# Optimization experiments

Measured on AMD Instinct MI355X. Metric: run time of the kernel, lower is better.

The kernel has to match this reference:

```python
import jax, jax.numpy as jnp
import numpy as np

B = 262144
HIST = 24
FORE = 20
HID = 256
# torch: tau_int = clamp(tau,1,18).long().item(); default tau=6.0 -> static 6 (host sync in torch)
TAU_INT = 6


def setup_inputs() -> dict:
    key = jax.random.key(0)
    ks = jax.random.split(key, 9)
    s = 0.1
    return {
        "history": jax.random.normal(ks[0], (B, HIST), jnp.float32),
        "enc_w1": jax.random.normal(ks[1], (HIST + FORE, HID), jnp.float32) * s,
        "enc_b1": jnp.zeros((HID,), jnp.float32),
        "enc_w2": jax.random.normal(ks[2], (HID, HID), jnp.float32) * s,
        "enc_b2": jnp.zeros((HID,), jnp.float32),
        "cor_w1": jax.random.normal(ks[3], (HID, HID), jnp.float32) * s,
        "cor_b1": jnp.zeros((HID,), jnp.float32),
        "cor_w2": jax.random.normal(ks[4], (HID, FORE), jnp.float32) * s,
        "cor_b2": jnp.zeros((FORE,), jnp.float32),
        "alpha": jnp.float32(0.2),
        "beta": jnp.float32(0.3),
        "gamma": jnp.float32(0.01),
        "tau": jnp.float32(6.0),
        "lambda_mix": jnp.float32(0.5),
    }


def _physics_core(history, alpha, beta, gamma, steps):
    a = jax.nn.sigmoid(alpha)
    b = jax.nn.sigmoid(beta)
    g = jnp.abs(gamma)
    T0 = history[:, -1]                      # [B]
    buf0 = history[:, -TAU_INT:].T           # [tau, B]; buf0[0] = history[:, -tau]

    def step(carry, _):
        T, buf = carry
        T_delayed = buf[0]
        T_new = T - a * T - b * T_delayed - g * T ** 3
        buf = jnp.concatenate([buf[1:], T_new[None, :]], axis=0)
        return (T_new, buf), T_new

    _, preds = jax.lax.scan(step, (T0, buf0), None, length=steps)
    return preds.T                            # [B, steps]


def reference(history, enc_w1, enc_b1, enc_w2, enc_b2,
              cor_w1, cor_b1, cor_w2, cor_b2,
              alpha, beta, gamma, tau, lambda_mix):
    T_physics = _physics_core(history, alpha, beta, gamma, FORE)   # [B, FORE]
    combined = jnp.concatenate([history, T_physics], axis=1)       # [B, HIST+FORE]
    h = jnp.tanh(combined @ enc_w1 + enc_b1)
    features = jnp.tanh(h @ enc_w2 + enc_b2)
    c = jnp.tanh(features @ cor_w1 + cor_b1)
    T_soft = c @ cor_w2 + cor_b2                                   # [B, FORE]
    lam = jax.nn.sigmoid(lambda_mix)
    T_pred = T_physics + lam * T_soft
    return (T_pred, T_physics, T_soft)
```

## Files before the change

### kernel.cpp

```cpp
#include <hip/hip_runtime.h>
#include <hip/hip_bf16.h>

#define NROWS 262144
#define HISTC 24
#define FOREC 20

typedef __bf16        v8bf __attribute__((ext_vector_type(8)));
typedef float         v4f  __attribute__((ext_vector_type(4)));
typedef unsigned int  v4u  __attribute__((ext_vector_type(4)));
typedef unsigned int  v2u  __attribute__((ext_vector_type(2)));

#define WS_WT1_OFF 64
#define WT1_ELEMS 16384
#define WT2_ELEMS 65536
#define WT3_ELEMS 65536
#define WT4_ELEMS 8192

__device__ __forceinline__ unsigned short f2bf(float x) {
    unsigned u = __builtin_bit_cast(unsigned, x);
    u += 0x7FFFu + ((u >> 16) & 1u);
    return (unsigned short)(u >> 16);
}

__device__ __forceinline__ unsigned pack2bf(float a, float b) {
    unsigned ua = __builtin_bit_cast(unsigned, a);
    unsigned ub = __builtin_bit_cast(unsigned, b);
    ua += 0x7FFFu + ((ua >> 16) & 1u);
    ub += 0x7FFFu + ((ub >> 16) & 1u);
    return (ua >> 16) | (ub & 0xFFFF0000u);
}

__device__ __forceinline__ float fast_tanh(float x) {
    float t = x * 2.885390081777927f;
    float p = __builtin_amdgcn_exp2f(t);
    float r = __builtin_amdgcn_rcpf(p + 1.0f);
    return __builtin_fmaf(-2.0f, r, 1.0f);
}

__global__ void prep_kernel(const float* __restrict__ w1, const float* __restrict__ w2,
                            const float* __restrict__ w3, const float* __restrict__ w4,
                            const float* __restrict__ alpha, const float* __restrict__ beta,
                            const float* __restrict__ gamma, const float* __restrict__ lmix,
                            unsigned char* __restrict__ ws)
{
    if (blockIdx.x == 608) {
        int t = threadIdx.x;
        float* wsf = (float*)ws;
        if (t == 0) wsf[0] = 1.0f / (1.0f + expf(-alpha[0]));
        else if (t == 1) wsf[1] = 1.0f / (1.0f + expf(-beta[0]));
        else if (t == 2) wsf[2] = fabsf(gamma[0]);
        else if (t == 3) wsf[3] = 1.0f / (1.0f + expf(-lmix[0]));
        return;
    }
    int idx = blockIdx.x * 256 + threadIdx.x;
    const float* src;
    int KT, Kreal, Nreal, srcN, local;
    unsigned short* dst = (unsigned short*)(ws + WS_WT1_OFF);
    if (idx < WT1_ELEMS) {
        local = idx; src = w1; KT = 2; Kreal = 44; Nreal = 256; srcN = 256;
    } else if (idx < WT1_ELEMS + WT2_ELEMS) {
        local = idx - WT1_ELEMS; dst += WT1_ELEMS;
        src = w2; KT = 8; Kreal = 256; Nreal = 256; srcN = 256;
    } else if (idx < WT1_ELEMS + WT2_ELEMS + WT3_ELEMS) {
        local = idx - (WT1_ELEMS + WT2_ELEMS); dst += WT1_ELEMS + WT2_ELEMS;
        src = w3; KT = 8; Kreal = 256; Nreal = 256; srcN = 256;
    } else {
        local = idx - (WT1_ELEMS + WT2_ELEMS + WT3_ELEMS);
        dst += WT1_ELEMS + WT2_ELEMS + WT3_ELEMS;
        src = w4; KT = 8; Kreal = 256; Nreal = 20; srcN = 20;
    }
    int j   = local & 7;
    int L   = (local >> 3) & 63;
    int blk = local >> 9;
    int kt = blk % KT, nt = blk / KT;
    int cc = L & 15,  qq = L >> 4;
    int feat = nt * 16 + cc;
    int k    = kt * 32 + qq * 8 + j;
    float v = (k < Kreal && feat < Nreal) ? src[k * srcN + feat] : 0.0f;
    dst[local] = f2bf(v);
}

template<int KT, int SIN>
__device__ __forceinline__ void layer123(unsigned short* buf,
        const unsigned short* __restrict__ wsw, const float* __restrict__ bias,
        int w, int c, int q, int lane)
{
    const v4u* wp = (const v4u*)wsw;
    v4u a[4][KT];
#pragma unroll
    for (int ft = 0; ft < 4; ++ft)
#pragma unroll
        for (int kt = 0; kt < KT; ++kt)
            a[ft][kt] = wp[((w * 4 + ft) * KT + kt) * 64 + lane];

    v4f acc[4][4];
#pragma unroll
    for (int ft = 0; ft < 4; ++ft)
#pragma unroll
        for (int st = 0; st < 4; ++st) {
            v4f z = {0.0f, 0.0f, 0.0f, 0.0f};
            acc[ft][st] = z;
        }

#pragma unroll
    for (int st = 0; st < 4; ++st)
#pragma unroll
        for (int kt = 0; kt < KT; ++kt) {
            v4u braw = *(const v4u*)&buf[(st * 16 + c) * SIN + kt * 32 + q * 8];
            v8bf bb = __builtin_bit_cast(v8bf, braw);
#pragma unroll
            for (int ft = 0; ft < 4; ++ft)
                acc[ft][st] = __builtin_amdgcn_mfma_f32_16x16x32_bf16(
                    __builtin_bit_cast(v8bf, a[ft][kt]), bb, acc[ft][st], 0, 0, 0);
        }

    __syncthreads();

#pragma unroll
    for (int ft = 0; ft < 4; ++ft) {
        v4f bi = *(const v4f*)&bias[w * 64 + ft * 16 + q * 4];
#pragma unroll
        for (int st = 0; st < 4; ++st) {
            float x0 = fast_tanh(acc[ft][st][0] + bi[0]);
            float x1 = fast_tanh(acc[ft][st][1] + bi[1]);
            float x2 = fast_tanh(acc[ft][st][2] + bi[2]);
            float x3 = fast_tanh(acc[ft][st][3] + bi[3]);
            v2u d; d[0] = pack2bf(x0, x1); d[1] = pack2bf(x2, x3);
            *(v2u*)&buf[(st * 16 + c) * 264 + w * 64 + ft * 16 + q * 4] = d;
        }
    }
    __syncthreads();
}

__global__ __launch_bounds__(256, 2) void fused_kernel(
    const float* __restrict__ history,
    const float* __restrict__ eb1, const float* __restrict__ eb2,
    const float* __restrict__ cb1, const float* __restrict__ cb2,
    const unsigned char* __restrict__ ws, float* __restrict__ out)
{
    __shared__ unsigned short buf[64 * 264];
    __shared__ float tp[64 * 20];

    const int tid  = threadIdx.x;
    const int w    = tid >> 6;
    const int lane = tid & 63;
    const int c    = lane & 15;
    const int q    = lane >> 4;
    const int row0 = blockIdx.x << 6;
    const float* wsf = (const float*)ws;
    const unsigned short* wt1 = (const unsigned short*)(ws + WS_WT1_OFF);
    const unsigned short* wt2 = wt1 + WT1_ELEMS;
    const unsigned short* wt3 = wt2 + WT2_ELEMS;
    const unsigned short* wt4 = wt3 + WT3_ELEMS;

    float* hist = (float*)&buf[8192];

#pragma unroll
    for (int i = 0; i < 6; ++i) {
        int e = tid + i * 256;
        int r = e / 24, cc = e - r * 24;
        hist[r * 25 + cc] = history[row0 * 24 + e];
    }
    __syncthreads();

#pragma unroll
    for (int i = 0; i < 6; ++i) {
        int e = tid + i * 256;
        int r = e / 24, cc = e - r * 24;
        buf[r * 72 + cc] = f2bf(hist[r * 25 + cc]);
    }
#pragma unroll
    for (int i = 0; i < 5; ++i) {
        int e = tid + i * 256;
        int r = e / 20, cc = e - r * 20;
        buf[r * 72 + 44 + cc] = 0;
    }
    if (tid < 64) {
        float pa = wsf[0], pb = wsf[1], pg = wsf[2];
        float d0 = hist[tid * 25 + 18], d1 = hist[tid * 25 + 19], d2 = hist[tid * 25 + 20];
        float d3 = hist[tid * 25 + 21], d4 = hist[tid * 25 + 22], d5 = hist[tid * 25 + 23];
        float T = d5;
#pragma unroll
        for (int s = 0; s < 20; ++s) {
            float t3 = T * T * T;
            float Tn = T - pa * T;
            Tn = Tn - pb * d0;
            Tn = Tn - pg * t3;
            tp[tid * 20 + s] = Tn;
            buf[tid * 72 + 24 + s] = f2bf(Tn);
            d0 = d1; d1 = d2; d2 = d3; d3 = d4; d4 = d5; d5 = Tn;
            T = Tn;
        }
    }
    __syncthreads();

    layer123<2, 72>(buf, wt1, eb1, w, c, q, lane);
    layer123<8, 264>(buf, wt2, eb2, w, c, q, lane);
    layer123<8, 264>(buf, wt3, cb1, w, c, q, lane);

    const v4u* wp4 = (const v4u*)wt4;
    v4u a4[2][8];
#pragma unroll
    for (int ft = 0; ft < 2; ++ft)
#pragma unroll
        for (int kt = 0; kt < 8; ++kt)
            a4[ft][kt] = wp4[(ft * 8 + kt) * 64 + lane];
    v4f acc0 = {0.0f, 0.0f, 0.0f, 0.0f}, acc1 = {0.0f, 0.0f, 0.0f, 0.0f};
#pragma unroll
    for (int kt = 0; kt < 8; ++kt) {
        v4u braw = *(const v4u*)&buf[(w * 16 + c) * 264 + kt * 32 + q * 8];
        v8bf bb = __builtin_bit_cast(v8bf, braw);
        acc0 = __builtin_amdgcn_mfma_f32_16x16x32_bf16(__builtin_bit_cast(v8bf, a4[0][kt]), bb, acc0, 0, 0, 0);
        acc1 = __builtin_amdgcn_mfma_f32_16x16x32_bf16(__builtin_bit_cast(v8bf, a4[1][kt]), bb, acc1, 0, 0, 0);
    }

    const float lam = wsf[3];
    const long sample = (long)row0 + w * 16 + c;
    float* outP = out;
    float* outF = out + (long)NROWS * 20;
    float* outS = out + (long)NROWS * 40;
    {
        v4f bi  = *(const v4f*)&cb2[q * 4];
        v4f tph = *(const v4f*)&tp[(w * 16 + c) * 20 + q * 4];
        v4f ts, pr;
#pragma unroll
        for (int r = 0; r < 4; ++r) {
            ts[r] = acc0[r] + bi[r];
            pr[r] = tph[r] + lam * ts[r];
        }
        *(v4f*)&outS[sample * 20 + q * 4] = ts;
        *(v4f*)&outP[sample * 20 + q * 4] = pr;
        *(v4f*)&outF[sample * 20 + q * 4] = tph;
    }
    if (q == 0) {
        v4f bi  = *(const v4f*)&cb2[16];
        v4f tph = *(const v4f*)&tp[(w * 16 + c) * 20 + 16];
        v4f ts, pr;
#pragma unroll
        for (int r = 0; r < 4; ++r) {
            ts[r] = acc1[r] + bi[r];
            pr[r] = tph[r] + lam * ts[r];
        }
        *(v4f*)&outS[sample * 20 + 16] = ts;
        *(v4f*)&outP[sample * 20 + 16] = pr;
        *(v4f*)&outF[sample * 20 + 16] = tph;
    }
}

extern "C" void kernel_launch(void* const* d_in, const int* in_sizes, int n_in,
                              void* d_out, int out_size, void* d_ws, size_t ws_size,
                              hipStream_t stream)
{
    const float* history = (const float*)d_in[0];
    const float* enc_w1  = (const float*)d_in[1];
    const float* enc_b1  = (const float*)d_in[2];
    const float* enc_w2  = (const float*)d_in[3];
    const float* enc_b2  = (const float*)d_in[4];
    const float* cor_w1  = (const float*)d_in[5];
    const float* cor_b1  = (const float*)d_in[6];
    const float* cor_w2  = (const float*)d_in[7];
    const float* cor_b2  = (const float*)d_in[8];
    const float* alpha   = (const float*)d_in[9];
    const float* beta    = (const float*)d_in[10];
    const float* gamma   = (const float*)d_in[11];
    const float* lmix    = (const float*)d_in[13];

    prep_kernel<<<609, 256, 0, stream>>>(enc_w1, enc_w2, cor_w1, cor_w2,
                                         alpha, beta, gamma, lmix,
                                         (unsigned char*)d_ws);
    fused_kernel<<<NROWS / 64, 256, 0, stream>>>(history, enc_b1, enc_b2, cor_b1, cor_b2,
                                                 (const unsigned char*)d_ws, (float*)d_out);
}
```

Before: 220.0 us.

## Use 512-thread blocks with streamed weight fragments and vectorized weight prep

```diff
diff --git a/kernel.cpp b/kernel.cpp
--- a/kernel.cpp
+++ b/kernel.cpp
@@ -43,7 +43,7 @@
                             const float* __restrict__ gamma, const float* __restrict__ lmix,
                             unsigned char* __restrict__ ws)
 {
-    if (blockIdx.x == 608) {
+    if (blockIdx.x == 76) {
         int t = threadIdx.x;
         float* wsf = (float*)ws;
         if (t == 0) wsf[0] = 1.0f / (1.0f + expf(-alpha[0]));
@@ -52,7 +52,7 @@
         else if (t == 3) wsf[3] = 1.0f / (1.0f + expf(-lmix[0]));
         return;
     }
-    int idx = blockIdx.x * 256 + threadIdx.x;
+    int idx = (blockIdx.x * 256 + threadIdx.x) * 8;
     const float* src;
     int KT, Kreal, Nreal, srcN, local;
     unsigned short* dst = (unsigned short*)(ws + WS_WT1_OFF);
@@ -69,15 +69,25 @@
         dst += WT1_ELEMS + WT2_ELEMS + WT3_ELEMS;
         src = w4; KT = 8; Kreal = 256; Nreal = 20; srcN = 20;
     }
-    int j   = local & 7;
     int L   = (local >> 3) & 63;
     int blk = local >> 9;
     int kt = blk % KT, nt = blk / KT;
     int cc = L & 15,  qq = L >> 4;
     int feat = nt * 16 + cc;
-    int k    = kt * 32 + qq * 8 + j;
-    float v = (k < Kreal && feat < Nreal) ? src[k * srcN + feat] : 0.0f;
-    dst[local] = f2bf(v);
+    int kbase = kt * 32 + qq * 8;
+    unsigned short tmp[8];
+#pragma unroll
+    for (int j = 0; j < 8; ++j) {
+        int k = kbase + j;
+        float v = (k < Kreal && feat < Nreal) ? src[k * srcN + feat] : 0.0f;
+        tmp[j] = f2bf(v);
+    }
+    v4u pk;
+    pk[0] = tmp[0] | ((unsigned)tmp[1] << 16);
+    pk[1] = tmp[2] | ((unsigned)tmp[3] << 16);
+    pk[2] = tmp[4] | ((unsigned)tmp[5] << 16);
+    pk[3] = tmp[6] | ((unsigned)tmp[7] << 16);
+    *(v4u*)&dst[local] = pk;
 }
 
 template<int KT, int SIN>
@@ -86,39 +96,35 @@
         int w, int c, int q, int lane)
 {
     const v4u* wp = (const v4u*)wsw;
-    v4u a[4][KT];
-#pragma unroll
-    for (int ft = 0; ft < 4; ++ft)
-#pragma unroll
-        for (int kt = 0; kt < KT; ++kt)
-            a[ft][kt] = wp[((w * 4 + ft) * KT + kt) * 64 + lane];
-
-    v4f acc[4][4];
-#pragma unroll
-    for (int ft = 0; ft < 4; ++ft)
+    v4f acc[2][4];
+#pragma unroll
+    for (int ft = 0; ft < 2; ++ft)
 #pragma unroll
         for (int st = 0; st < 4; ++st) {
             v4f z = {0.0f, 0.0f, 0.0f, 0.0f};
             acc[ft][st] = z;
         }
 
-#pragma unroll
-    for (int st = 0; st < 4; ++st)
-#pragma unroll
-        for (int kt = 0; kt < KT; ++kt) {
+#pragma unroll 2
+    for (int kt = 0; kt < KT; ++kt) {
+        v4u a0 = wp[((w * 2 + 0) * KT + kt) * 64 + lane];
+        v4u a1 = wp[((w * 2 + 1) * KT + kt) * 64 + lane];
+#pragma unroll
+        for (int st = 0; st < 4; ++st) {
             v4u braw = *(const v4u*)&buf[(st * 16 + c) * SIN + kt * 32 + q * 8];
             v8bf bb = __builtin_bit_cast(v8bf, braw);
-#pragma unroll
-            for (int ft = 0; ft < 4; ++ft)
-                acc[ft][st] = __builtin_amdgcn_mfma_f32_16x16x32_bf16(
-                    __builtin_bit_cast(v8bf, a[ft][kt]), bb, acc[ft][st], 0, 0, 0);
-        }
-
-    __syncthreads();
-
-#pragma unroll
-    for (int ft = 0; ft < 4; ++ft) {
-        v4f bi = *(const v4f*)&bias[w * 64 + ft * 16 + q * 4];
+            acc[0][st] = __builtin_amdgcn_mfma_f32_16x16x32_bf16(
+                __builtin_bit_cast(v8bf, a0), bb, acc[0][st], 0, 0, 0);
+            acc[1][st] = __builtin_amdgcn_mfma_f32_16x16x32_bf16(
+                __builtin_bit_cast(v8bf, a1), bb, acc[1][st], 0, 0, 0);
+        }
+    }
+
+    __syncthreads();
+
+#pragma unroll
+    for (int ft = 0; ft < 2; ++ft) {
+        v4f bi = *(const v4f*)&bias[w * 32 + ft * 16 + q * 4];
 #pragma unroll
         for (int st = 0; st < 4; ++st) {
             float x0 = fast_tanh(acc[ft][st][0] + bi[0]);
@@ -126,13 +132,13 @@
             float x2 = fast_tanh(acc[ft][st][2] + bi[2]);
             float x3 = fast_tanh(acc[ft][st][3] + bi[3]);
             v2u d; d[0] = pack2bf(x0, x1); d[1] = pack2bf(x2, x3);
-            *(v2u*)&buf[(st * 16 + c) * 264 + w * 64 + ft * 16 + q * 4] = d;
-        }
-    }
-    __syncthreads();
-}
-
-__global__ __launch_bounds__(256, 2) void fused_kernel(
+            *(v2u*)&buf[(st * 16 + c) * 264 + w * 32 + ft * 16 + q * 4] = d;
+        }
+    }
+    __syncthreads();
+}
+
+__global__ __launch_bounds__(512, 4) void fused_kernel(
     const float* __restrict__ history,
     const float* __restrict__ eb1, const float* __restrict__ eb2,
     const float* __restrict__ cb1, const float* __restrict__ cb2,
@@ -156,24 +162,26 @@
     float* hist = (float*)&buf[8192];
 
 #pragma unroll
-    for (int i = 0; i < 6; ++i) {
-        int e = tid + i * 256;
+    for (int i = 0; i < 3; ++i) {
+        int e = tid + i * 512;
         int r = e / 24, cc = e - r * 24;
         hist[r * 25 + cc] = history[row0 * 24 + e];
     }
     __syncthreads();
 
 #pragma unroll
-    for (int i = 0; i < 6; ++i) {
-        int e = tid + i * 256;
+    for (int i = 0; i < 3; ++i) {
+        int e = tid + i * 512;
         int r = e / 24, cc = e - r * 24;
         buf[r * 72 + cc] = f2bf(hist[r * 25 + cc]);
     }
 #pragma unroll
-    for (int i = 0; i < 5; ++i) {
-        int e = tid + i * 256;
-        int r = e / 20, cc = e - r * 20;
-        buf[r * 72 + 44 + cc] = 0;
+    for (int i = 0; i < 3; ++i) {
+        int e = tid + i * 512;
+        if (e < 1280) {
+            int r = e / 20, cc = e - r * 20;
+            buf[r * 72 + 44 + cc] = 0;
+        }
     }
     if (tid < 64) {
         float pa = wsf[0], pb = wsf[1], pg = wsf[2];
@@ -198,52 +206,37 @@
     layer123<8, 264>(buf, wt2, eb2, w, c, q, lane);
     layer123<8, 264>(buf, wt3, cb1, w, c, q, lane);
 
+    const int ft4 = w >> 2;
+    const int st4 = w & 3;
     const v4u* wp4 = (const v4u*)wt4;
-    v4u a4[2][8];
-#pragma unroll
-    for (int ft = 0; ft < 2; ++ft)
-#pragma unroll
-        for (int kt = 0; kt < 8; ++kt)
-            a4[ft][kt] = wp4[(ft * 8 + kt) * 64 + lane];
-    v4f acc0 = {0.0f, 0.0f, 0.0f, 0.0f}, acc1 = {0.0f, 0.0f, 0.0f, 0.0f};
-#pragma unroll
+    v4f acc4 = {0.0f, 0.0f, 0.0f, 0.0f};
+#pragma unroll 2
     for (int kt = 0; kt < 8; ++kt) {
-        v4u braw = *(const v4u*)&buf[(w * 16 + c) * 264 + kt * 32 + q * 8];
+        v4u a = wp4[(ft4 * 8 + kt) * 64 + lane];
+        v4u braw = *(const v4u*)&buf[(st4 * 16 + c) * 264 + kt * 32 + q * 8];
         v8bf bb = __builtin_bit_cast(v8bf, braw);
-        acc0 = __builtin_amdgcn_mfma_f32_16x16x32_bf16(__builtin_bit_cast(v8bf, a4[0][kt]), bb, acc0, 0, 0, 0);
-        acc1 = __builtin_amdgcn_mfma_f32_16x16x32_bf16(__builtin_bit_cast(v8bf, a4[1][kt]), bb, acc1, 0, 0, 0);
+        acc4 = __builtin_amdgcn_mfma_f32_16x16x32_bf16(
+            __builtin_bit_cast(v8bf, a), bb, acc4, 0, 0, 0);
     }
 
     const float lam = wsf[3];
-    const long sample = (long)row0 + w * 16 + c;
+    const long sample = (long)row0 + st4 * 16 + c;
     float* outP = out;
     float* outF = out + (long)NROWS * 20;
     float* outS = out + (long)NROWS * 40;
-    {
-        v4f bi  = *(const v4f*)&cb2[q * 4];
-        v4f tph = *(const v4f*)&tp[(w * 16 + c) * 20 + q * 4];
+    const int f0 = ft4 * 16 + q * 4;
+    if (f0 < 20) {
+        v4f bi  = *(const v4f*)&cb2[f0];
+        v4f tph = *(const v4f*)&tp[(st4 * 16 + c) * 20 + f0];
         v4f ts, pr;
 #pragma unroll
         for (int r = 0; r < 4; ++r) {
-            ts[r] = acc0[r] + bi[r];
+            ts[r] = acc4[r] + bi[r];
             pr[r] = tph[r] + lam * ts[r];
         }
-        *(v4f*)&outS[sample * 20 + q * 4] = ts;
-        *(v4f*)&outP[sample * 20 + q * 4] = pr;
-        *(v4f*)&outF[sample * 20 + q * 4] = tph;
-    }
-    if (q == 0) {
-        v4f bi  = *(const v4f*)&cb2[16];
-        v4f tph = *(const v4f*)&tp[(w * 16 + c) * 20 + 16];
-        v4f ts, pr;
-#pragma unroll
-        for (int r = 0; r < 4; ++r) {
-            ts[r] = acc1[r] + bi[r];
-            pr[r] = tph[r] + lam * ts[r];
-        }
-        *(v4f*)&outS[sample * 20 + 16] = ts;
-        *(v4f*)&outP[sample * 20 + 16] = pr;
-        *(v4f*)&outF[sample * 20 + 16] = tph;
+        *(v4f*)&outS[sample * 20 + f0] = ts;
+        *(v4f*)&outP[sample * 20 + f0] = pr;
+        *(v4f*)&outF[sample * 20 + f0] = tph;
     }
 }
 
@@ -265,9 +258,9 @@
     const float* gamma   = (const float*)d_in[11];
     const float* lmix    = (const float*)d_in[13];
 
-    prep_kernel<<<609, 256, 0, stream>>>(enc_w1, enc_w2, cor_w1, cor_w2,
-                                         alpha, beta, gamma, lmix,
-                                         (unsigned char*)d_ws);
-    fused_kernel<<<NROWS / 64, 256, 0, stream>>>(history, enc_b1, enc_b2, cor_b1, cor_b2,
+    prep_kernel<<<77, 256, 0, stream>>>(enc_w1, enc_w2, cor_w1, cor_w2,
+                                        alpha, beta, gamma, lmix,
+                                        (unsigned char*)d_ws);
+    fused_kernel<<<NROWS / 64, 512, 0, stream>>>(history, enc_b1, enc_b2, cor_b1, cor_b2,
                                                  (const unsigned char*)d_ws, (float*)d_out);
 }
```

Result: no change. 216.6 us (-1.6%).
